# Kernel tuning notes

Hardware: AMD Instinct MI355X
Metric: run time of the kernel (lower is better)

The kernel has to match this reference:

```python
import jax, jax.numpy as jnp
import numpy as np

NEG = -1e30  # finite stand-in for -inf so softmax grads stay clean


def setup_inputs() -> dict:
    key = jax.random.key(0)
    k1, k2 = jax.random.split(key)
    C, D = 8192, 512
    gt_class_embeddings = jax.random.normal(k1, (C, D), dtype=jnp.float32)
    w = jax.random.normal(k2, (C, D), dtype=jnp.float32)
    return {"gt_class_embeddings": gt_class_embeddings, "w": w}


def reference(gt_class_embeddings, w):
    # L2-normalize class embeddings, cosine-similarity matrix S (diag == 1)
    G = gt_class_embeddings / jnp.linalg.norm(gt_class_embeddings, axis=-1, keepdims=True)
    S = G @ G.T  # [C, C]
    C = S.shape[0]
    off_diag = ~jnp.eye(C, dtype=bool)

    # seSoftmax: per-row softmax over entries != 1 (off-diagonal); diagonal stays 1
    P = jax.nn.softmax(jnp.where(off_diag, S, NEG), axis=-1)
    S2 = jnp.where(off_diag, P, 1.0)

    # argsort(-S2)[1] == most similar (diag value 1 always ranks first),
    # argsort(-S2)[-1] == least similar == row min (softmax values < 1)
    ms = jnp.argmax(jnp.where(off_diag, S2, NEG), axis=-1)  # [C]
    ls = jnp.argmin(jnp.where(off_diag, S2, -NEG), axis=-1)  # [C]

    rows = jnp.arange(C)
    margin = S2[rows, ms] - S2[rows, ls]  # [C]

    d_ms = jnp.sqrt(jnp.sum((w - w[ms]) ** 2, axis=-1))  # [C]
    d_ls = jnp.sqrt(jnp.sum((w - w[ls]) ** 2, axis=-1))  # [C]

    loss = jnp.mean(jnp.maximum(0.0, d_ms - d_ls + margin))
    return loss
```

## Files before the change

kernel.cpp:

```cpp
#include <hip/hip_runtime.h>
#include <math.h>

#define CDIM 8192
#define DDIM 512
#define NEGF -3.0e38f
#define POSF  3.0e38f

#define BM 128
#define NSLOT (CDIM / BM)

typedef __attribute__((ext_vector_type(8))) short bf16x8;
typedef __attribute__((ext_vector_type(4))) float f32x4;

__device__ __forceinline__ unsigned short f2bf(float x) {
    unsigned int u = __float_as_uint(x);
    u += 0x7fffu + ((u >> 16) & 1u);
    return (unsigned short)(u >> 16);
}
__device__ __forceinline__ float bf2f(unsigned short h) {
    return __uint_as_float(((unsigned int)h) << 16);
}
__device__ __forceinline__ void gld16(const void* g, void* l) {
    __builtin_amdgcn_global_load_lds(
        (__attribute__((address_space(1))) void*)(void*)g,
        (__attribute__((address_space(3))) void*)l, 16, 0, 0);
}

__global__ __launch_bounds__(256) void k_prep(const float* __restrict__ g,
                                              unsigned short* __restrict__ hi,
                                              unsigned short* __restrict__ lo) {
    const int wave = threadIdx.x >> 6;
    const int lane = threadIdx.x & 63;
    const int row = blockIdx.x * 4 + wave;
    const float4* src = (const float4*)(g + (size_t)row * DDIM);
    const float4 a = src[lane * 2];
    const float4 b = src[lane * 2 + 1];
    float s = a.x * a.x + a.y * a.y + a.z * a.z + a.w * a.w +
              b.x * b.x + b.y * b.y + b.z * b.z + b.w * b.w;
#pragma unroll
    for (int m = 1; m < 64; m <<= 1) s += __shfl_xor(s, m, 64);
    const float rn = rsqrtf(s);
    const float y[8] = {a.x * rn, a.y * rn, a.z * rn, a.w * rn,
                        b.x * rn, b.y * rn, b.z * rn, b.w * rn};
    unsigned int hv[4], lv[4];
#pragma unroll
    for (int i = 0; i < 4; ++i) {
        const unsigned short h0 = f2bf(y[2 * i]);
        const unsigned short h1 = f2bf(y[2 * i + 1]);
        const unsigned short l0 = f2bf(y[2 * i] - bf2f(h0));
        const unsigned short l1 = f2bf(y[2 * i + 1] - bf2f(h1));
        hv[i] = (unsigned int)h0 | ((unsigned int)h1 << 16);
        lv[i] = (unsigned int)l0 | ((unsigned int)l1 << 16);
    }
    uint4* dh = (uint4*)(hi + (size_t)row * DDIM + lane * 8);
    uint4* dl = (uint4*)(lo + (size_t)row * DDIM + lane * 8);
    *dh = make_uint4(hv[0], hv[1], hv[2], hv[3]);
    *dl = make_uint4(lv[0], lv[1], lv[2], lv[3]);
}

__device__ __constant__ unsigned char OSUP[28] = {
    1, 2, 10,   3, 11, 19,   4, 12, 20,   28, 5, 13,
    21, 29, 37, 6,   14, 22, 30, 38,   46, 7, 15, 23,   31, 39, 47, 55};

__global__ __launch_bounds__(256, 3) void k_simstats(
    const unsigned short* __restrict__ ghi, const unsigned short* __restrict__ glo,
    float* __restrict__ pmax, float* __restrict__ pmin, float* __restrict__ pZ,
    int* __restrict__ pamax, int* __restrict__ pamin) {
    const int bid = blockIdx.x;
    const int xcd = bid & 7;
    const int off = bid >> 3;
    int I, J;
    if (xcd < 4) {
        if (off < 72) {
            const int s = xcd * 2 + (off >= 36);
            const int u = (off >= 36) ? off - 36 : off;
            int jj = 0;
            while ((jj + 1) * (jj + 2) / 2 <= u) ++jj;
            const int ii = u - jj * (jj + 1) / 2;
            I = s * 8 + ii; J = s * 8 + jj;
        } else {
            const int sup = (off - 72) >> 6;
            const int u = (off - 72) & 63;
            const int code = OSUP[xcd * 3 + sup];
            I = (code >> 3) * 8 + (u & 7);
            J = (code & 7) * 8 + (u >> 3);
        }
    } else {
        if (off >= 256) return;
        const int sup = off >> 6;
        const int u = off & 63;
        const int code = OSUP[12 + (xcd - 4) * 4 + sup];
        I = (code >> 3) * 8 + (u & 7);
        J = (code & 7) * 8 + (u >> 3);
    }

    __shared__ unsigned short SH[4 * BM * 32];
    unsigned short* Ahi = SH;
    unsigned short* Alo = SH + 4096;
    unsigned short* Bhi = SH + 8192;
    unsigned short* Blo = SH + 12288;
    const int t = threadIdx.x;
    const int wave = t >> 6;
    const int lane = t & 63;
    const int lanelo = lane & 15;
    const int quad = lane >> 4;
    const int wr = wave & 1;
    const int wc = wave >> 1;

    const int srow = t >> 2;
    const int scolb = ((t & 3) ^ ((t >> 3) & 3)) << 4;
    char* lAh = (char*)Ahi + t * 16;
    char* lAl = (char*)Alo + t * 16;
    char* lBh = (char*)Bhi + t * 16;
    char* lBl = (char*)Blo + t * 16;

    const int fsl = (quad ^ ((lanelo >> 1) & 3)) << 3;
    const int aoff = (wr * 64 + lanelo) * 32 + fsl;
    const int boff = (wc * 64 + lanelo) * 32 + fsl;

    float* rm  = (float*)SH;
    float* rz  = rm + 256;
    float* rmn = rz + 256;
    int*   ra  = (int*)(rmn + 256);
    int*   ran = ra + 256;
    float* cm  = (float*)Bhi;
    float* cz  = cm + 256;
    float* cmn = cz + 256;
    int*   ca  = (int*)(cmn + 256);
    int*   can = ca + 256;

    const int i0 = I * BM;
    const int j0 = J * BM;
    const bool isdiag = (I == J);

    f32x4 acc[4][4];
#pragma unroll
    for (int rt = 0; rt < 4; ++rt)
#pragma unroll
        for (int ct = 0; ct < 4; ++ct)
            acc[rt][ct] = (f32x4){0.f, 0.f, 0.f, 0.f};

    const char* baseAh = (const char*)ghi + (size_t)(i0 + srow) * 1024 + scolb;
    const char* baseAl = (const char*)glo + (size_t)(i0 + srow) * 1024 + scolb;
    const char* baseBh = (const char*)ghi + (size_t)(j0 + srow) * 1024 + scolb;
    const char* baseBl = (const char*)glo + (size_t)(j0 + srow) * 1024 + scolb;

    for (int k0 = 0; k0 < DDIM; k0 += 32) {
        __syncthreads();
#pragma unroll
        for (int q = 0; q < 2; ++q) {
            const size_t roff = (size_t)q * 64 * 1024 + k0 * 2;
            gld16(baseAh + roff, lAh + q * 4096);
            gld16(baseAl + roff, lAl + q * 4096);
            gld16(baseBh + roff, lBh + q * 4096);
            gld16(baseBl + roff, lBl + q * 4096);
        }
        __syncthreads();
        bf16x8 ah[4], al[4];
#pragma unroll
        for (int rt = 0; rt < 4; ++rt) {
            ah[rt] = *(const bf16x8*)&Ahi[aoff + rt * 512];
            al[rt] = *(const bf16x8*)&Alo[aoff + rt * 512];
        }
#pragma unroll
        for (int ct = 0; ct < 4; ++ct) {
            const bf16x8 bh = *(const bf16x8*)&Bhi[boff + ct * 512];
            const bf16x8 bl = *(const bf16x8*)&Blo[boff + ct * 512];
#pragma unroll
            for (int rt = 0; rt < 4; ++rt) {
                acc[rt][ct] = __builtin_amdgcn_mfma_f32_16x16x32_bf16(
                    ah[rt], bh, acc[rt][ct], 0, 0, 0);
                acc[rt][ct] = __builtin_amdgcn_mfma_f32_16x16x32_bf16(
                    ah[rt], bl, acc[rt][ct], 0, 0, 0);
                acc[rt][ct] = __builtin_amdgcn_mfma_f32_16x16x32_bf16(
                    al[rt], bh, acc[rt][ct], 0, 0, 0);
            }
        }
    }

    __syncthreads();

#pragma unroll
    for (int rt = 0; rt < 4; ++rt) {
#pragma unroll
        for (int r = 0; r < 4; ++r) {
            const int lrow = wr * 64 + rt * 16 + quad * 4 + r;
            float tmax = NEGF; int targ = 0;
            float tmin = POSF; int targn = 0;
            if (isdiag) {
                const int gi = i0 + lrow;
#pragma unroll
                for (int ct = 0; ct < 4; ++ct) {
                    const int gj = j0 + wc * 64 + ct * 16 + lanelo;
                    const float v = acc[rt][ct][r];
                    const bool dg = (gj == gi);
                    const float vM = dg ? NEGF : v;
                    const float vm = dg ? POSF : v;
                    if (vM > tmax) { tmax = vM; targ = gj; }
                    if (vm < tmin) { tmin = vm; targn = gj; }
                }
            } else {
#pragma unroll
                for (int ct = 0; ct < 4; ++ct) {
                    const int gj = j0 + wc * 64 + ct * 16 + lanelo;
                    const float v = acc[rt][ct][r];
                    if (v > tmax) { tmax = v; targ = gj; }
                    if (v < tmin) { tmin = v; targn = gj; }
                }
            }
#pragma unroll
            for (int msk = 1; msk < 16; msk <<= 1) {
                const float v2 = __shfl_xor(tmax, msk, 64);
                const int i2 = __shfl_xor(targ, msk, 64);
                if (v2 > tmax) { tmax = v2; targ = i2; }
                const float v3 = __shfl_xor(tmin, msk, 64);
                const int i3 = __shfl_xor(targn, msk, 64);
                if (v3 < tmin) { tmin = v3; targn = i3; }
            }
            if (lanelo == 0) {
                const int o = wc * 128 + lrow;
                rm[o] = tmax; rmn[o] = tmin;
                ra[o] = targ; ran[o] = targn;
            }
        }
    }

    if (!isdiag) {
#pragma unroll
        for (int ct = 0; ct < 4; ++ct) {
            const int lcol = wc * 64 + ct * 16 + lanelo;
            float tmax = NEGF; int targ = 0;
            float tmin = POSF; int targn = 0;
#pragma unroll
            for (int rt = 0; rt < 4; ++rt)
#pragma unroll
                for (int r = 0; r < 4; ++r) {
                    const int gi = i0 + wr * 64 + rt * 16 + quad * 4 + r;
                    const float v = acc[rt][ct][r];
                    if (v > tmax) { tmax = v; targ = gi; }
                    if (v < tmin) { tmin = v; targn = gi; }
                }
#pragma unroll
            for (int msk = 16; msk < 64; msk <<= 1) {
                const float m2 = __shfl_xor(tmax, msk, 64);
                const int i2 = __shfl_xor(targ, msk, 64);
                if (m2 > tmax) { tmax = m2; targ = i2; }
                const float mn2 = __shfl_xor(tmin, msk, 64);
                const int in2 = __shfl_xor(targn, msk, 64);
                if (mn2 < tmin) { tmin = mn2; targn = in2; }
            }
            if (quad == 0) {
                const int o = wr * 128 + lcol;
                cm[o] = tmax; cmn[o] = tmin;
                ca[o] = targ; can[o] = targn;
            }
        }
    }

#pragma unroll
    for (int rt = 0; rt < 4; ++rt)
#pragma unroll
        for (int ct = 0; ct < 4; ++ct)
#pragma unroll
            for (int r = 0; r < 4; ++r)
                acc[rt][ct][r] = __expf(acc[rt][ct][r] - 1.f);
    if (isdiag && wr == wc) {
#pragma unroll
        for (int rt = 0; rt < 4; ++rt)
#pragma unroll
            for (int r = 0; r < 4; ++r)
                if (lanelo == quad * 4 + r) acc[rt][rt][r] = 0.f;
    }

#pragma unroll
    for (int rt = 0; rt < 4; ++rt)
#pragma unroll
        for (int r = 0; r < 4; ++r) {
            float s = acc[rt][0][r] + acc[rt][1][r] +
                      acc[rt][2][r] + acc[rt][3][r];
#pragma unroll
            for (int msk = 1; msk < 16; msk <<= 1) s += __shfl_xor(s, msk, 64);
            if (lanelo == 0)
                rz[wc * 128 + wr * 64 + rt * 16 + quad * 4 + r] = s;
        }

    if (!isdiag) {
#pragma unroll
        for (int ct = 0; ct < 4; ++ct) {
            float s = 0.f;
#pragma unroll
            for (int rt = 0; rt < 4; ++rt)
                s += acc[rt][ct][0] + acc[rt][ct][1] +
                     acc[rt][ct][2] + acc[rt][ct][3];
#pragma unroll
            for (int msk = 16; msk < 64; msk <<= 1) s += __shfl_xor(s, msk, 64);
            if (quad == 0)
                cz[wr * 128 + wc * 64 + ct * 16 + lanelo] = s;
        }
    }

    __syncthreads();

    if (t < BM) {
        const float m0 = rm[t], m1 = rm[128 + t];
        float vmax = m0; int imax = ra[t];
        if (m1 > vmax) { vmax = m1; imax = ra[128 + t]; }
        float vmin = rmn[t]; int imin = ran[t];
        if (rmn[128 + t] < vmin) { vmin = rmn[128 + t]; imin = ran[128 + t]; }
        const size_t o = (size_t)J * CDIM + i0 + t;
        pmax[o] = vmax; pmin[o] = vmin; pZ[o] = rz[t] + rz[128 + t];
        pamax[o] = imax; pamin[o] = imin;
    } else if (!isdiag) {
        const int tt = t - BM;
        const float m0 = cm[tt], m1 = cm[128 + tt];
        float vmax = m0; int imax = ca[tt];
        if (m1 > vmax) { vmax = m1; imax = ca[128 + tt]; }
        float vmin = cmn[tt]; int imin = can[tt];
        if (cmn[128 + tt] < vmin) { vmin = cmn[128 + tt]; imin = can[128 + tt]; }
        const size_t o = (size_t)I * CDIM + j0 + tt;
        pmax[o] = vmax; pmin[o] = vmin; pZ[o] = cz[tt] + cz[128 + tt];
        pamax[o] = imax; pamin[o] = imin;
    }
}

__global__ __launch_bounds__(256) void k_lossc(
    const float* __restrict__ pmax, const float* __restrict__ pmin,
    const float* __restrict__ pZ, const int* __restrict__ pamax,
    const int* __restrict__ pamin, const float* __restrict__ w,
    float* __restrict__ vals) {
    const int wave = threadIdx.x >> 6;
    const int lane = threadIdx.x & 63;
    const int row = blockIdx.x * 4 + wave;
    const size_t o = (size_t)lane * CDIM + row;
    float v = pmax[o]; int a = pamax[o];
    float u = pmin[o]; int b = pamin[o];
    float z = pZ[o];
#pragma unroll
    for (int msk = 1; msk < 64; msk <<= 1) {
        const float v2 = __shfl_xor(v, msk, 64);
        const int i2 = __shfl_xor(a, msk, 64);
        if (v2 > v) { v = v2; a = i2; }
        const float v3 = __shfl_xor(u, msk, 64);
        const int i3 = __shfl_xor(b, msk, 64);
        if (v3 < u) { u = v3; b = i3; }
        z += __shfl_xor(z, msk, 64);
    }
    const float margin = (1.f - __expf(u - v)) * __expf(v - 1.f) / z;
    const int jm = a, jl = b;

    const float4* wi = (const float4*)(w + (size_t)row * DDIM);
    const float4* wm = (const float4*)(w + (size_t)jm * DDIM);
    const float4* wl = (const float4*)(w + (size_t)jl * DDIM);
    float sm = 0.f, sl = 0.f;
#pragma unroll
    for (int h = 0; h < 2; ++h) {
        const int idx = h * 64 + lane;
        const float4 x = wi[idx];
        const float4 y = wm[idx];
        const float4 c = wl[idx];
        float d;
        d = x.x - y.x; sm = fmaf(d, d, sm);
        d = x.y - y.y; sm = fmaf(d, d, sm);
        d = x.z - y.z; sm = fmaf(d, d, sm);
        d = x.w - y.w; sm = fmaf(d, d, sm);
        d = x.x - c.x; sl = fmaf(d, d, sl);
        d = x.y - c.y; sl = fmaf(d, d, sl);
        d = x.z - c.z; sl = fmaf(d, d, sl);
        d = x.w - c.w; sl = fmaf(d, d, sl);
    }
#pragma unroll
    for (int msk = 1; msk < 64; msk <<= 1) {
        sm += __shfl_xor(sm, msk, 64);
        sl += __shfl_xor(sl, msk, 64);
    }
    if (lane == 0) {
        const float val = sqrtf(sm) - sqrtf(sl) + margin;
        vals[row] = val > 0.f ? val : 0.f;
    }
}

__global__ __launch_bounds__(256) void k_final(const float* __restrict__ vals,
                                               float* __restrict__ out) {
    __shared__ float red[256];
    float s = 0.f;
    for (int i = threadIdx.x; i < CDIM; i += 256) s += vals[i];
    red[threadIdx.x] = s;
    __syncthreads();
#pragma unroll
    for (int k = 128; k > 0; k >>= 1) {
        if (threadIdx.x < (unsigned)k) red[threadIdx.x] += red[threadIdx.x + k];
        __syncthreads();
    }
    if (threadIdx.x == 0) out[0] = red[0] * (1.0f / CDIM);
}

extern "C" void kernel_launch(void* const* d_in, const int* in_sizes, int n_in,
                              void* d_out, int out_size, void* d_ws, size_t ws_size,
                              hipStream_t stream) {
    const float* g = (const float*)d_in[0];
    const float* w = (const float*)d_in[1];
    float* out = (float*)d_out;

    unsigned short* ghi = (unsigned short*)d_ws;
    unsigned short* glo = ghi + (size_t)CDIM * DDIM;
    float* p = (float*)(glo + (size_t)CDIM * DDIM);
    float* pmax = p;      p += (size_t)NSLOT * CDIM;
    float* pmin = p;      p += (size_t)NSLOT * CDIM;
    float* pZ = p;        p += (size_t)NSLOT * CDIM;
    int* pamax = (int*)p; p += (size_t)NSLOT * CDIM;
    int* pamin = (int*)p; p += (size_t)NSLOT * CDIM;
    float* vals = p;      p += CDIM;

    k_prep<<<CDIM / 4, 256, 0, stream>>>(g, ghi, glo);
    k_simstats<<<2112, 256, 0, stream>>>(ghi, glo, pmax, pmin, pZ, pamax, pamin);
    k_lossc<<<CDIM / 4, 256, 0, stream>>>(pmax, pmin, pZ, pamax, pamin, w, vals);
    k_final<<<1, 256, 0, stream>>>(vals, out);
}
```

Measured before the change: 230.9 us.

## Double-buffer LDS tiles in similarity GEMM to overlap global loads with MFMA

Replaces the single-buffered K loop with a two-stage LDS ping-pong, issuing the next K-slice's global-to-LDS loads before computing the current slice. Partial vmcnt waits and raw s_barrier calls replace the paired __syncthreads. s_setprio raises wave priority during MFMA work. LDS use doubles to 64KB, and launch bounds drop from 3 to 2 blocks per SM, which reduces occupancy.

After: 249.6 us. 1.08x slower.

```diff
diff --git a/kernel.cpp b/kernel.cpp
--- a/kernel.cpp
+++ b/kernel.cpp
@@ -62,7 +62,7 @@
     1, 2, 10,   3, 11, 19,   4, 12, 20,   28, 5, 13,
     21, 29, 37, 6,   14, 22, 30, 38,   46, 7, 15, 23,   31, 39, 47, 55};
 
-__global__ __launch_bounds__(256, 3) void k_simstats(
+__global__ __launch_bounds__(256, 2) void k_simstats(
     const unsigned short* __restrict__ ghi, const unsigned short* __restrict__ glo,
     float* __restrict__ pmax, float* __restrict__ pmin, float* __restrict__ pZ,
     int* __restrict__ pamax, int* __restrict__ pamin) {
@@ -94,11 +94,7 @@
         J = (code & 7) * 8 + (u >> 3);
     }
 
-    __shared__ unsigned short SH[4 * BM * 32];
-    unsigned short* Ahi = SH;
-    unsigned short* Alo = SH + 4096;
-    unsigned short* Bhi = SH + 8192;
-    unsigned short* Blo = SH + 12288;
+    __shared__ unsigned short SH[2 * 4 * BM * 32];
     const int t = threadIdx.x;
     const int wave = t >> 6;
     const int lane = t & 63;
@@ -109,10 +105,6 @@
 
     const int srow = t >> 2;
     const int scolb = ((t & 3) ^ ((t >> 3) & 3)) << 4;
-    char* lAh = (char*)Ahi + t * 16;
-    char* lAl = (char*)Alo + t * 16;
-    char* lBh = (char*)Bhi + t * 16;
-    char* lBl = (char*)Blo + t * 16;
 
     const int fsl = (quad ^ ((lanelo >> 1) & 3)) << 3;
     const int aoff = (wr * 64 + lanelo) * 32 + fsl;
@@ -123,7 +115,7 @@
     float* rmn = rz + 256;
     int*   ra  = (int*)(rmn + 256);
     int*   ran = ra + 256;
-    float* cm  = (float*)Bhi;
+    float* cm  = (float*)(SH + 8192);
     float* cz  = cm + 256;
     float* cmn = cz + 256;
     int*   ca  = (int*)(cmn + 256);
@@ -145,27 +137,29 @@
     const char* baseBh = (const char*)ghi + (size_t)(j0 + srow) * 1024 + scolb;
     const char* baseBl = (const char*)glo + (size_t)(j0 + srow) * 1024 + scolb;
 
-    for (int k0 = 0; k0 < DDIM; k0 += 32) {
-        __syncthreads();
+    auto STAGE = [&](int ks, int b) {
+        char* const d = (char*)SH + b * 32768 + t * 16;
+        const size_t cb = (size_t)ks * 64;
 #pragma unroll
         for (int q = 0; q < 2; ++q) {
-            const size_t roff = (size_t)q * 64 * 1024 + k0 * 2;
-            gld16(baseAh + roff, lAh + q * 4096);
-            gld16(baseAl + roff, lAl + q * 4096);
-            gld16(baseBh + roff, lBh + q * 4096);
-            gld16(baseBl + roff, lBl + q * 4096);
-        }
-        __syncthreads();
+            const size_t roff = (size_t)q * 64 * 1024 + cb;
+            gld16(baseAh + roff, d + q * 4096);
+            gld16(baseAl + roff, d + 8192 + q * 4096);
+            gld16(baseBh + roff, d + 16384 + q * 4096);
+            gld16(baseBl + roff, d + 24576 + q * 4096);
+        }
+    };
+    auto COMPUTE = [&](const unsigned short* base) {
         bf16x8 ah[4], al[4];
 #pragma unroll
         for (int rt = 0; rt < 4; ++rt) {
-            ah[rt] = *(const bf16x8*)&Ahi[aoff + rt * 512];
-            al[rt] = *(const bf16x8*)&Alo[aoff + rt * 512];
+            ah[rt] = *(const bf16x8*)&base[aoff + rt * 512];
+            al[rt] = *(const bf16x8*)&base[4096 + aoff + rt * 512];
         }
 #pragma unroll
         for (int ct = 0; ct < 4; ++ct) {
-            const bf16x8 bh = *(const bf16x8*)&Bhi[boff + ct * 512];
-            const bf16x8 bl = *(const bf16x8*)&Blo[boff + ct * 512];
+            const bf16x8 bh = *(const bf16x8*)&base[8192 + boff + ct * 512];
+            const bf16x8 bl = *(const bf16x8*)&base[12288 + boff + ct * 512];
 #pragma unroll
             for (int rt = 0; rt < 4; ++rt) {
                 acc[rt][ct] = __builtin_amdgcn_mfma_f32_16x16x32_bf16(
@@ -176,9 +170,30 @@
                     al[rt], bh, acc[rt][ct], 0, 0, 0);
             }
         }
-    }
-
-    __syncthreads();
+    };
+
+    STAGE(0, 0);
+    for (int ks = 0; ks < 15; ++ks) {
+        STAGE(ks + 1, (ks + 1) & 1);
+        asm volatile("s_waitcnt vmcnt(8)" ::: "memory");
+        __builtin_amdgcn_s_barrier();
+        asm volatile("" ::: "memory");
+        __builtin_amdgcn_s_setprio(1);
+        COMPUTE(SH + (ks & 1) * 16384);
+        __builtin_amdgcn_s_setprio(0);
+        asm volatile("s_waitcnt lgkmcnt(0)" ::: "memory");
+        __builtin_amdgcn_s_barrier();
+        asm volatile("" ::: "memory");
+    }
+    asm volatile("s_waitcnt vmcnt(0)" ::: "memory");
+    __builtin_amdgcn_s_barrier();
+    asm volatile("" ::: "memory");
+    __builtin_amdgcn_s_setprio(1);
+    COMPUTE(SH + 16384);
+    __builtin_amdgcn_s_setprio(0);
+    asm volatile("s_waitcnt lgkmcnt(0)" ::: "memory");
+    __builtin_amdgcn_s_barrier();
+    asm volatile("" ::: "memory");
 
 #pragma unroll
     for (int rt = 0; rt < 4; ++rt) {
```

## Load MFMA operands directly from global memory instead of staging through LDS

Applied to the files above, without the earlier changes.

The GEMM main loop no longer stages A/B hi/lo tiles into shared memory with global_load_lds and barriers. Each wave now reads its bf16x8 fragments straight from global memory (relying on L2/L1) in a fully unrolled 16-step k loop. LDS is cut down to small reduction buffers, and launch bounds drop to 2 blocks per SIMD to allow more registers. This removes the per-iteration syncthreads and the LDS traffic, but each fragment is fetched redundantly across waves and latency is hidden only by register prefetch across the unrolled loop.

Result: slower. 428.8 us (+85.7%).

```diff
diff --git a/kernel.cpp b/kernel.cpp
--- a/kernel.cpp
+++ b/kernel.cpp
@@ -19,11 +19,6 @@
 }
 __device__ __forceinline__ float bf2f(unsigned short h) {
     return __uint_as_float(((unsigned int)h) << 16);
-}
-__device__ __forceinline__ void gld16(const void* g, void* l) {
-    __builtin_amdgcn_global_load_lds(
-        (__attribute__((address_space(1))) void*)(void*)g,
-        (__attribute__((address_space(3))) void*)l, 16, 0, 0);
 }
 
 __global__ __launch_bounds__(256) void k_prep(const float* __restrict__ g,
@@ -62,7 +57,7 @@
     1, 2, 10,   3, 11, 19,   4, 12, 20,   28, 5, 13,
     21, 29, 37, 6,   14, 22, 30, 38,   46, 7, 15, 23,   31, 39, 47, 55};
 
-__global__ __launch_bounds__(256, 3) void k_simstats(
+__global__ __launch_bounds__(256, 2) void k_simstats(
     const unsigned short* __restrict__ ghi, const unsigned short* __restrict__ glo,
     float* __restrict__ pmax, float* __restrict__ pmin, float* __restrict__ pZ,
     int* __restrict__ pamax, int* __restrict__ pamin) {
@@ -94,11 +89,11 @@
         J = (code & 7) * 8 + (u >> 3);
     }
 
-    __shared__ unsigned short SH[4 * BM * 32];
-    unsigned short* Ahi = SH;
-    unsigned short* Alo = SH + 4096;
-    unsigned short* Bhi = SH + 8192;
-    unsigned short* Blo = SH + 12288;
+    __shared__ float rm[256];  __shared__ float rz[256];
+    __shared__ float rmn[256]; __shared__ int ra[256]; __shared__ int ran[256];
+    __shared__ float cm[256];  __shared__ float cz[256];
+    __shared__ float cmn[256]; __shared__ int ca[256]; __shared__ int can[256];
+
     const int t = threadIdx.x;
     const int wave = t >> 6;
     const int lane = t & 63;
@@ -107,28 +102,6 @@
     const int wr = wave & 1;
     const int wc = wave >> 1;
 
-    const int srow = t >> 2;
-    const int scolb = ((t & 3) ^ ((t >> 3) & 3)) << 4;
-    char* lAh = (char*)Ahi + t * 16;
-    char* lAl = (char*)Alo + t * 16;
-    char* lBh = (char*)Bhi + t * 16;
-    char* lBl = (char*)Blo + t * 16;
-
-    const int fsl = (quad ^ ((lanelo >> 1) & 3)) << 3;
-    const int aoff = (wr * 64 + lanelo) * 32 + fsl;
-    const int boff = (wc * 64 + lanelo) * 32 + fsl;
-
-    float* rm  = (float*)SH;
-    float* rz  = rm + 256;
-    float* rmn = rz + 256;
-    int*   ra  = (int*)(rmn + 256);
-    int*   ran = ra + 256;
-    float* cm  = (float*)Bhi;
-    float* cz  = cm + 256;
-    float* cmn = cz + 256;
-    int*   ca  = (int*)(cmn + 256);
-    int*   can = ca + 256;
-
     const int i0 = I * BM;
     const int j0 = J * BM;
     const bool isdiag = (I == J);
@@ -140,45 +113,36 @@
         for (int ct = 0; ct < 4; ++ct)
             acc[rt][ct] = (f32x4){0.f, 0.f, 0.f, 0.f};
 
-    const char* baseAh = (const char*)ghi + (size_t)(i0 + srow) * 1024 + scolb;
-    const char* baseAl = (const char*)glo + (size_t)(i0 + srow) * 1024 + scolb;
-    const char* baseBh = (const char*)ghi + (size_t)(j0 + srow) * 1024 + scolb;
-    const char* baseBl = (const char*)glo + (size_t)(j0 + srow) * 1024 + scolb;
-
-    for (int k0 = 0; k0 < DDIM; k0 += 32) {
-        __syncthreads();
-#pragma unroll
-        for (int q = 0; q < 2; ++q) {
-            const size_t roff = (size_t)q * 64 * 1024 + k0 * 2;
-            gld16(baseAh + roff, lAh + q * 4096);
-            gld16(baseAl + roff, lAl + q * 4096);
-            gld16(baseBh + roff, lBh + q * 4096);
-            gld16(baseBl + roff, lBl + q * 4096);
-        }
-        __syncthreads();
-        bf16x8 ah[4], al[4];
+    const size_t aoff = (size_t)(i0 + wr * 64 + lanelo) * 1024 + quad * 16;
+    const size_t boff = (size_t)(j0 + wc * 64 + lanelo) * 1024 + quad * 16;
+    const char* const Ah = (const char*)ghi + aoff;
+    const char* const Al = (const char*)glo + aoff;
+    const char* const Bh = (const char*)ghi + boff;
+    const char* const Bl = (const char*)glo + boff;
+
+#pragma unroll
+    for (int k = 0; k < 16; ++k) {
+        bf16x8 ah[4], al[4], bh[4], bl[4];
 #pragma unroll
         for (int rt = 0; rt < 4; ++rt) {
-            ah[rt] = *(const bf16x8*)&Ahi[aoff + rt * 512];
-            al[rt] = *(const bf16x8*)&Alo[aoff + rt * 512];
-        }
-#pragma unroll
-        for (int ct = 0; ct < 4; ++ct) {
-            const bf16x8 bh = *(const bf16x8*)&Bhi[boff + ct * 512];
-            const bf16x8 bl = *(const bf16x8*)&Blo[boff + ct * 512];
+            const int d = rt * 16 * 1024 + k * 64;
+            ah[rt] = *(const bf16x8*)(Ah + d);
+            al[rt] = *(const bf16x8*)(Al + d);
+            bh[rt] = *(const bf16x8*)(Bh + d);
+            bl[rt] = *(const bf16x8*)(Bl + d);
+        }
+#pragma unroll
+        for (int ct = 0; ct < 4; ++ct)
 #pragma unroll
             for (int rt = 0; rt < 4; ++rt) {
                 acc[rt][ct] = __builtin_amdgcn_mfma_f32_16x16x32_bf16(
-                    ah[rt], bh, acc[rt][ct], 0, 0, 0);
+                    ah[rt], bh[ct], acc[rt][ct], 0, 0, 0);
                 acc[rt][ct] = __builtin_amdgcn_mfma_f32_16x16x32_bf16(
-                    ah[rt], bl, acc[rt][ct], 0, 0, 0);
+                    ah[rt], bl[ct], acc[rt][ct], 0, 0, 0);
                 acc[rt][ct] = __builtin_amdgcn_mfma_f32_16x16x32_bf16(
-                    al[rt], bh, acc[rt][ct], 0, 0, 0);
-            }
-        }
-    }
-
-    __syncthreads();
+                    al[rt], bh[ct], acc[rt][ct], 0, 0, 0);
+            }
+    }
 
 #pragma unroll
     for (int rt = 0; rt < 4; ++rt) {
@@ -242,9 +206,9 @@
                 }
 #pragma unroll
             for (int msk = 16; msk < 64; msk <<= 1) {
-                const float m2 = __shfl_xor(tmax, msk, 64);
+                const float m2v = __shfl_xor(tmax, msk, 64);
                 const int i2 = __shfl_xor(targ, msk, 64);
-                if (m2 > tmax) { tmax = m2; targ = i2; }
+                if (m2v > tmax) { tmax = m2v; targ = i2; }
                 const float mn2 = __shfl_xor(tmin, msk, 64);
                 const int in2 = __shfl_xor(targn, msk, 64);
                 if (mn2 < tmin) { tmin = mn2; targn = in2; }
```

## Fuse all stages into one persistent cooperative kernel with atomic tile scheduling

Applied to the files above, without the earlier changes.

Replaces the four separate launches (prep, simstats, lossc, final) with one cooperative persistent kernel of 768 blocks that uses grid-wide syncs between phases. The similarity tiles are handed out dynamically through per-XCD atomic counters, which keeps the existing XCD-aware tile mapping. The aim is to remove launch gaps and tail effects between kernels. In exchange it adds grid-sync costs, limits occupancy to 3 blocks per CU, and falls back to the old multi-kernel path if the cooperative launch fails.

Result: slower. 661.2 us (+186.3%).

```diff
diff --git a/kernel.cpp b/kernel.cpp
--- a/kernel.cpp
+++ b/kernel.cpp
@@ -1,5 +1,8 @@
 #include <hip/hip_runtime.h>
+#include <hip/hip_cooperative_groups.h>
 #include <math.h>
+
+namespace cg = cooperative_groups;
 
 #define CDIM 8192
 #define DDIM 512
@@ -26,50 +29,11 @@
         (__attribute__((address_space(3))) void*)l, 16, 0, 0);
 }
 
-__global__ __launch_bounds__(256) void k_prep(const float* __restrict__ g,
-                                              unsigned short* __restrict__ hi,
-                                              unsigned short* __restrict__ lo) {
-    const int wave = threadIdx.x >> 6;
-    const int lane = threadIdx.x & 63;
-    const int row = blockIdx.x * 4 + wave;
-    const float4* src = (const float4*)(g + (size_t)row * DDIM);
-    const float4 a = src[lane * 2];
-    const float4 b = src[lane * 2 + 1];
-    float s = a.x * a.x + a.y * a.y + a.z * a.z + a.w * a.w +
-              b.x * b.x + b.y * b.y + b.z * b.z + b.w * b.w;
-#pragma unroll
-    for (int m = 1; m < 64; m <<= 1) s += __shfl_xor(s, m, 64);
-    const float rn = rsqrtf(s);
-    const float y[8] = {a.x * rn, a.y * rn, a.z * rn, a.w * rn,
-                        b.x * rn, b.y * rn, b.z * rn, b.w * rn};
-    unsigned int hv[4], lv[4];
-#pragma unroll
-    for (int i = 0; i < 4; ++i) {
-        const unsigned short h0 = f2bf(y[2 * i]);
-        const unsigned short h1 = f2bf(y[2 * i + 1]);
-        const unsigned short l0 = f2bf(y[2 * i] - bf2f(h0));
-        const unsigned short l1 = f2bf(y[2 * i + 1] - bf2f(h1));
-        hv[i] = (unsigned int)h0 | ((unsigned int)h1 << 16);
-        lv[i] = (unsigned int)l0 | ((unsigned int)l1 << 16);
-    }
-    uint4* dh = (uint4*)(hi + (size_t)row * DDIM + lane * 8);
-    uint4* dl = (uint4*)(lo + (size_t)row * DDIM + lane * 8);
-    *dh = make_uint4(hv[0], hv[1], hv[2], hv[3]);
-    *dl = make_uint4(lv[0], lv[1], lv[2], lv[3]);
-}
-
 __device__ __constant__ unsigned char OSUP[28] = {
     1, 2, 10,   3, 11, 19,   4, 12, 20,   28, 5, 13,
     21, 29, 37, 6,   14, 22, 30, 38,   46, 7, 15, 23,   31, 39, 47, 55};
 
-__global__ __launch_bounds__(256, 3) void k_simstats(
-    const unsigned short* __restrict__ ghi, const unsigned short* __restrict__ glo,
-    float* __restrict__ pmax, float* __restrict__ pmin, float* __restrict__ pZ,
-    int* __restrict__ pamax, int* __restrict__ pamin) {
-    const int bid = blockIdx.x;
-    const int xcd = bid & 7;
-    const int off = bid >> 3;
-    int I, J;
+__device__ __forceinline__ void tile_map(int xcd, int off, int& I, int& J) {
     if (xcd < 4) {
         if (off < 72) {
             const int s = xcd * 2 + (off >= 36);
@@ -86,20 +50,54 @@
             J = (code & 7) * 8 + (u >> 3);
         }
     } else {
-        if (off >= 256) return;
         const int sup = off >> 6;
         const int u = off & 63;
         const int code = OSUP[12 + (xcd - 4) * 4 + sup];
         I = (code >> 3) * 8 + (u & 7);
         J = (code & 7) * 8 + (u >> 3);
     }
-
-    __shared__ unsigned short SH[4 * BM * 32];
+}
+
+
+__device__ __forceinline__ void prep_row(const float* __restrict__ g,
+                                         unsigned short* __restrict__ hi,
+                                         unsigned short* __restrict__ lo,
+                                         int row, int lane) {
+    const float4* src = (const float4*)(g + (size_t)row * DDIM);
+    const float4 a = src[lane * 2];
+    const float4 b = src[lane * 2 + 1];
+    float s = a.x * a.x + a.y * a.y + a.z * a.z + a.w * a.w +
+              b.x * b.x + b.y * b.y + b.z * b.z + b.w * b.w;
+#pragma unroll
+    for (int m = 1; m < 64; m <<= 1) s += __shfl_xor(s, m, 64);
+    const float rn = rsqrtf(s);
+    const float y[8] = {a.x * rn, a.y * rn, a.z * rn, a.w * rn,
+                        b.x * rn, b.y * rn, b.z * rn, b.w * rn};
+    unsigned int hv[4], lv[4];
+#pragma unroll
+    for (int i = 0; i < 4; ++i) {
+        const unsigned short h0 = f2bf(y[2 * i]);
+        const unsigned short h1 = f2bf(y[2 * i + 1]);
+        const unsigned short l0 = f2bf(y[2 * i] - bf2f(h0));
+        const unsigned short l1 = f2bf(y[2 * i + 1] - bf2f(h1));
+        hv[i] = (unsigned int)h0 | ((unsigned int)h1 << 16);
+        lv[i] = (unsigned int)l0 | ((unsigned int)l1 << 16);
+    }
+    uint4* dh = (uint4*)(hi + (size_t)row * DDIM + lane * 8);
+    uint4* dl = (uint4*)(lo + (size_t)row * DDIM + lane * 8);
+    *dh = make_uint4(hv[0], hv[1], hv[2], hv[3]);
+    *dl = make_uint4(lv[0], lv[1], lv[2], lv[3]);
+}
+
+__device__ __forceinline__ void simstats_tile(
+    const unsigned short* __restrict__ ghi, const unsigned short* __restrict__ glo,
+    float* __restrict__ pmax, float* __restrict__ pmin, float* __restrict__ pZ,
+    int* __restrict__ pamax, int* __restrict__ pamin,
+    unsigned short* SH, int I, int J, int t) {
     unsigned short* Ahi = SH;
     unsigned short* Alo = SH + 4096;
     unsigned short* Bhi = SH + 8192;
     unsigned short* Blo = SH + 12288;
-    const int t = threadIdx.x;
     const int wave = t >> 6;
     const int lane = t & 63;
     const int lanelo = lane & 15;
@@ -323,14 +321,11 @@
     }
 }
 
-__global__ __launch_bounds__(256) void k_lossc(
+__device__ __forceinline__ void lossc_row(
     const float* __restrict__ pmax, const float* __restrict__ pmin,
     const float* __restrict__ pZ, const int* __restrict__ pamax,
     const int* __restrict__ pamin, const float* __restrict__ w,
-    float* __restrict__ vals) {
-    const int wave = threadIdx.x >> 6;
-    const int lane = threadIdx.x & 63;
-    const int row = blockIdx.x * 4 + wave;
+    float* __restrict__ vals, int row, int lane) {
     const size_t o = (size_t)lane * CDIM + row;
     float v = pmax[o]; int a = pamax[o];
     float u = pmin[o]; int b = pamin[o];
@@ -379,19 +374,108 @@
     }
 }
 
+__device__ __forceinline__ void final_mean(const float* __restrict__ vals,
+                                           float* __restrict__ out,
+                                           float* red, int t) {
+    float s = 0.f;
+    for (int i = t; i < CDIM; i += 256) s += vals[i];
+    red[t] = s;
+    __syncthreads();
+#pragma unroll
+    for (int k = 128; k > 0; k >>= 1) {
+        if (t < k) red[t] += red[t + k];
+        __syncthreads();
+    }
+    if (t == 0) out[0] = red[0] * (1.0f / CDIM);
+}
+
+__global__ __launch_bounds__(256, 3) void k_fused(
+    const float* __restrict__ g, const float* __restrict__ w,
+    unsigned short* __restrict__ ghi, unsigned short* __restrict__ glo,
+    float* __restrict__ pmax, float* __restrict__ pmin, float* __restrict__ pZ,
+    int* __restrict__ pamax, int* __restrict__ pamin,
+    float* __restrict__ vals, int* __restrict__ ctr, float* __restrict__ out) {
+    __shared__ unsigned short SH[4 * BM * 32];
+    __shared__ int s_off;
+    const int t = threadIdx.x;
+    const int wave = t >> 6;
+    const int lane = t & 63;
+    const int bid = blockIdx.x;
+    const int xcd = bid & 7;
+    const int wglob = bid * 4 + wave;
+
+    if (bid == 0 && t < 8) ctr[t] = 0;
+#pragma unroll
+    for (int j = 0; j < 3; ++j) {
+        const int row = wglob + 3072 * j;
+        if (row < CDIM) prep_row(g, ghi, glo, row, lane);
+    }
+    __threadfence();
+    cg::this_grid().sync();
+
+    const int lim = (xcd < 4) ? 264 : 256;
+    while (true) {
+        __syncthreads();
+        if (t == 0) s_off = atomicAdd(&ctr[xcd], 1);
+        __syncthreads();
+        const int off = s_off;
+        if (off >= lim) break;
+        int I, J;
+        tile_map(xcd, off, I, J);
+        simstats_tile(ghi, glo, pmax, pmin, pZ, pamax, pamin, SH, I, J, t);
+    }
+    __threadfence();
+    cg::this_grid().sync();
+
+#pragma unroll
+    for (int j = 0; j < 3; ++j) {
+        const int row = wglob + 3072 * j;
+        if (row < CDIM) lossc_row(pmax, pmin, pZ, pamax, pamin, w, vals, row, lane);
+    }
+    __threadfence();
+    cg::this_grid().sync();
+
+    if (bid == 0) final_mean(vals, out, (float*)SH, t);
+}
+
+
+__global__ __launch_bounds__(256) void k_prep(const float* __restrict__ g,
+                                              unsigned short* __restrict__ hi,
+                                              unsigned short* __restrict__ lo) {
+    const int wave = threadIdx.x >> 6;
+    const int lane = threadIdx.x & 63;
+    prep_row(g, hi, lo, blockIdx.x * 4 + wave, lane);
+}
+
+__global__ __launch_bounds__(256, 3) void k_simstats(
+    const unsigned short* __restrict__ ghi, const unsigned short* __restrict__ glo,
+    float* __restrict__ pmax, float* __restrict__ pmin, float* __restrict__ pZ,
+    int* __restrict__ pamax, int* __restrict__ pamin) {
+    __shared__ unsigned short SH[4 * BM * 32];
+    const int bid = blockIdx.x;
+    const int xcd = bid & 7;
+    const int off = bid >> 3;
+    if (xcd >= 4 && off >= 256) return;
+    int I, J;
+    tile_map(xcd, off, I, J);
+    simstats_tile(ghi, glo, pmax, pmin, pZ, pamax, pamin, SH, I, J,
+                  (int)threadIdx.x);
+}
+
+__global__ __launch_bounds__(256) void k_lossc(
+    const float* __restrict__ pmax, const float* __restrict__ pmin,
+    const float* __restrict__ pZ, const int* __restrict__ pamax,
+    const int* __restrict__ pamin, const float* __restrict__ w,
+    float* __restrict__ vals) {
+    const int wave = threadIdx.x >> 6;
+    const int lane = threadIdx.x & 63;
+    lossc_row(pmax, pmin, pZ, pamax, pamin, w, vals, blockIdx.x * 4 + wave, lane);
+}
+
 __global__ __launch_bounds__(256) void k_final(const float* __restrict__ vals,
                                                float* __restrict__ out) {
     __shared__ float red[256];
-    float s = 0.f;
-    for (int i = threadIdx.x; i < CDIM; i += 256) s += vals[i];
-    red[threadIdx.x] = s;
-    __syncthreads();
-#pragma unroll
-    for (int k = 128; k > 0; k >>= 1) {
-        if (threadIdx.x < (unsigned)k) red[threadIdx.x] += red[threadIdx.x + k];
-        __syncthreads();
-    }
-    if (threadIdx.x == 0) out[0] = red[0] * (1.0f / CDIM);
+    final_mean(vals, out, red, (int)threadIdx.x);
 }
 
 extern "C" void kernel_launch(void* const* d_in, const int* in_sizes, int n_in,
@@ -410,9 +494,23 @@
     int* pamax = (int*)p; p += (size_t)NSLOT * CDIM;
     int* pamin = (int*)p; p += (size_t)NSLOT * CDIM;
     float* vals = p;      p += CDIM;
-
-    k_prep<<<CDIM / 4, 256, 0, stream>>>(g, ghi, glo);
-    k_simstats<<<2112, 256, 0, stream>>>(ghi, glo, pmax, pmin, pZ, pamax, pamin);
-    k_lossc<<<CDIM / 4, 256, 0, stream>>>(pmax, pmin, pZ, pamax, pamin, w, vals);
-    k_final<<<1, 256, 0, stream>>>(vals, out);
-}
+    int* ctr = (int*)p;
+
+    void* args[12];
+    args[0] = (void*)&g;     args[1] = (void*)&w;
+    args[2] = (void*)&ghi;   args[3] = (void*)&glo;
+    args[4] = (void*)&pmax;  args[5] = (void*)&pmin;
+    args[6] = (void*)&pZ;    args[7] = (void*)&pamax;
+    args[8] = (void*)&pamin; args[9] = (void*)&vals;
+    args[10] = (void*)&ctr;  args[11] = (void*)&out;
+
+    if (hipLaunchCooperativeKernel((const void*)k_fused, dim3(768), dim3(256),
+                                   args, 0, stream) != hipSuccess) {
+        k_prep<<<CDIM / 4, 256, 0, stream>>>(g, ghi, glo);
+        k_simstats<<<2112, 256, 0, stream>>>(ghi, glo, pmax, pmin, pZ,
+                                             pamax, pamin);
+        k_lossc<<<CDIM / 4, 256, 0, stream>>>(pmax, pmin, pZ, pamax, pamin,
+                                              w, vals);
+        k_final<<<1, 256, 0, stream>>>(vals, out);
+    }
+}
```
